# Performance work log

Hardware: AMD Instinct MI355X
Metric: run time of the kernel (lower is better)

Reference implementation:

```python
import jax, jax.numpy as jnp
import numpy as np

B, IN_UNITS, IN_CHANNELS, NUM_UNITS, UNIT_SIZE = 128, 32, 4096, 10, 16
NUM_ITER = 3


def setup_inputs() -> dict:
    key = jax.random.key(0)
    k1, k2 = jax.random.split(key)
    # x: primary-capsule output [B, in_units, in_channels]
    x = jax.random.normal(k1, (B, IN_UNITS, IN_CHANNELS), dtype=jnp.float32)
    # W: routing weights, torch param shape [1, C, J, D, K] with batch dim dropped
    W = jax.random.normal(k2, (IN_CHANNELS, NUM_UNITS, UNIT_SIZE, IN_UNITS), dtype=jnp.float32)
    return {"x": x, "W": W}


def reference(x, W):
    b_sz = x.shape[0]
    C, J = W.shape[0], W.shape[1]
    # torch: x.transpose(1,2) -> [B,C,K]; u_hat = W @ x -> [B,C,J,D,1]
    # u_hat[b,i,j,d] = sum_k W[i,j,d,k] * x[b,k,i]
    u_hat = jnp.einsum('ijdk,bki->bijd', W, x)  # [B, C, J, D]
    b_ij = jnp.zeros((C, J), dtype=x.dtype)
    v = None
    for _ in range(NUM_ITER):
        # faithful: softmax over dim=1 (in_channels axis), not over classes
        c_ij = jax.nn.softmax(b_ij, axis=0)               # [C, J]
        s = jnp.einsum('ij,bijd->bjd', c_ij, u_hat)        # [B, J, D]
        # faithful squash: original sums over dim=2 of [B,1,J,D,1] == class axis J
        mag_sq = jnp.sum(s * s, axis=1, keepdims=True)     # [B, 1, D]
        v = (mag_sq / (1.0 + mag_sq)) * (s / jnp.sqrt(mag_sq))
        # agreement: <u_hat, v> averaged over batch
        agree = jnp.einsum('bijd,bjd->ij', u_hat, v) / b_sz
        b_ij = b_ij + agree
    # torch returns v_j.squeeze(1): [B, J, D, 1]
    return v[:, :, :, None]
```

## Files before the change

### kernel.cpp

```cpp
#include <hip/hip_runtime.h>


typedef __attribute__((ext_vector_type(8))) __bf16 bf16x8;
typedef __attribute__((ext_vector_type(4))) float  f32x4;
typedef __attribute__((ext_vector_type(8))) unsigned short u16x8;
typedef __attribute__((ext_vector_type(4))) unsigned int  u32x4;

#define DI __device__ __forceinline__

DI float bf2f(unsigned short u){ unsigned int x = ((unsigned int)u) << 16; return __builtin_bit_cast(float, x); }
DI unsigned short f2bf(float f){
  unsigned int u = __builtin_bit_cast(unsigned int, f);
  u += 0x7fffu + ((u >> 16) & 1u);
  return (unsigned short)(u >> 16);
}
DI unsigned int cvtpk(float lo, float hi){
  unsigned int r;
  asm("v_cvt_pk_bf16_f32 %0, %1, %2" : "=v"(r) : "v"(lo), "v"(hi));
  return r;
}

constexpr int Ci = 4096, Kk = 32, Jj = 10, Dd = 16, Bb = 128;
constexpr int KI = Ci * Kk;
constexpr int JDt = Jj * Dd;
constexpr int NCH = 256, CK = 512;

constexpr size_t OFF_W2 = 0;
constexpr size_t SZ_W2  = (size_t)JDt * KI * 2;
constexpr size_t OFF_XT = OFF_W2 + SZ_W2;
constexpr size_t SZ_XT  = (size_t)KI * Bb * 2;
constexpr size_t OFF_BT = OFF_XT + SZ_XT;
constexpr size_t SZ_BT  = (size_t)Jj * Ci * 4;
constexpr size_t OFF_CT = OFF_BT + SZ_BT;
constexpr size_t OFF_VBT = OFF_CT + SZ_BT;
constexpr size_t SZ_VBT = (size_t)JDt * Bb * 2;
constexpr size_t OFF_SP = OFF_VBT + SZ_VBT;
constexpr size_t SZ_SP  = (size_t)NCH * Bb * JDt * 4;

__global__ __launch_bounds__(256) void pack_w(const float* __restrict__ W, unsigned short* __restrict__ w2){
  __shared__ float tile[128][65];
  const int mt = blockIdx.x % 80, it = blockIdx.x / 80;
  const int m0 = mt * 64, i0 = it * 128;
  #pragma unroll
  for(int u=0; u<8; u++){
    int e = threadIdx.x + 256*u;
    int il = e >> 4, q = e & 15;
    float4 v = *(const float4*)(W + (size_t)(i0+il)*5120 + m0 + q*4);
    tile[il][q*4+0]=v.x; tile[il][q*4+1]=v.y; tile[il][q*4+2]=v.z; tile[il][q*4+3]=v.w;
  }
  __syncthreads();
  #pragma unroll
  for(int u=0; u<4; u++){
    int e = threadIdx.x + 256*u;
    int ml = e >> 4, q = e & 15;
    u32x4 o;
    o[0]=cvtpk(tile[q*8+0][ml], tile[q*8+1][ml]);
    o[1]=cvtpk(tile[q*8+2][ml], tile[q*8+3][ml]);
    o[2]=cvtpk(tile[q*8+4][ml], tile[q*8+5][ml]);
    o[3]=cvtpk(tile[q*8+6][ml], tile[q*8+7][ml]);
    *(u32x4*)(w2 + (size_t)(m0+ml)*Ci + i0 + q*8) = o;
  }
}

__global__ __launch_bounds__(256) void pack_xt(const float* __restrict__ x, unsigned short* __restrict__ xT,
                                               float* __restrict__ bT){
  __shared__ float tile[128][65];
  const int bid = blockIdx.x;
  if(bid >= 2048){
    ((f32x4*)bT)[(bid-2048)*256 + threadIdx.x] = f32x4{0.f,0.f,0.f,0.f};
    return;
  }
  const int ki0 = bid * 64;
  #pragma unroll
  for(int u=0; u<8; u++){
    int e = threadIdx.x + 256*u;
    int bl = e >> 4, q = e & 15;
    float4 v = *(const float4*)(x + (size_t)bl*KI + ki0 + q*4);
    tile[bl][q*4+0]=v.x; tile[bl][q*4+1]=v.y; tile[bl][q*4+2]=v.z; tile[bl][q*4+3]=v.w;
  }
  __syncthreads();
  #pragma unroll
  for(int u=0; u<4; u++){
    int e = threadIdx.x + 256*u;
    int kil = e >> 4, g = e & 15;
    u32x4 o;
    o[0]=cvtpk(tile[g*8+0][kil], tile[g*8+1][kil]);
    o[1]=cvtpk(tile[g*8+2][kil], tile[g*8+3][kil]);
    o[2]=cvtpk(tile[g*8+4][kil], tile[g*8+5][kil]);
    o[3]=cvtpk(tile[g*8+6][kil], tile[g*8+7][kil]);
    *(u32x4*)(xT + (size_t)(ki0+kil)*Bb + g*8) = o;
  }
}

__global__ __launch_bounds__(256) void softmax_k(const float* __restrict__ bT, float* __restrict__ cT){
  const int j = blockIdx.x, tid = threadIdx.x, lane = tid & 63, wid = tid >> 6;
  __shared__ float red[4];
  float vals[16];
  float mx = -3.4e38f;
  #pragma unroll
  for(int u=0; u<16; u++){ vals[u] = bT[j*Ci + tid + 256*u]; mx = fmaxf(mx, vals[u]); }
  #pragma unroll
  for(int o=32; o>0; o>>=1) mx = fmaxf(mx, __shfl_xor(mx, o));
  if(lane == 0) red[wid] = mx;
  __syncthreads();
  mx = fmaxf(fmaxf(red[0],red[1]), fmaxf(red[2],red[3]));
  float sm = 0.f;
  #pragma unroll
  for(int u=0; u<16; u++){ vals[u] = expf(vals[u]-mx); sm += vals[u]; }
  #pragma unroll
  for(int o=32; o>0; o>>=1) sm += __shfl_xor(sm, o);
  __syncthreads();
  if(lane == 0) red[wid] = sm;
  __syncthreads();
  sm = red[0]+red[1]+red[2]+red[3];
  float inv = 1.0f / sm;
  #pragma unroll
  for(int u=0; u<16; u++) cT[j*Ci + tid + 256*u] = vals[u]*inv;
}

__global__ __launch_bounds__(512) void s_pass(const float* __restrict__ x,
                                              const unsigned short* __restrict__ w2,
                                              const float* __restrict__ cT,
                                              float* __restrict__ spart){
  __shared__ unsigned short xs[2][128*64];
  __shared__ unsigned short wsm[2][160*64];
  const int tid = threadIdx.x, lane = tid & 63, wid = tid >> 6;
  const int wb = wid & 3, wj = wid >> 2;
  const int ki0 = blockIdx.x * CK;
  const float cu = 1.0f/4096.0f;

  const int xb_ = tid >> 3, xsg = tid & 7;
  f32x4 acc[2][5];
  #pragma unroll
  for(int m=0;m<2;m++)
    #pragma unroll
    for(int n=0;n<5;n++) acc[m][n] = f32x4{0.f,0.f,0.f,0.f};

  float4 xv[4]; u16x8 wv[3]; float4 cv[3][2];

  #define S_LOAD(STEP) { \
    const int kb = ki0 + (STEP)*64; \
    const float* xr = x + (size_t)xb_*KI + kb + xsg*8; \
    xv[0]=*(const float4*)xr; xv[1]=*(const float4*)(xr+4); \
    const float* xr2 = xr + (size_t)64*KI; \
    xv[2]=*(const float4*)xr2; xv[3]=*(const float4*)(xr2+4); \
    const int ib = kb & (Ci-1); \
    _Pragma("unroll") \
    for(int u=0; u<3; u++){ int e = tid + 512*u; if(e < 1280){ \
      int jd = e>>3, sg = e&7; \
      wv[u] = *(const u16x8*)(w2 + (size_t)jd*KI + kb + sg*8); \
      if(cT){ const float* cp = cT + (jd>>4)*Ci + ib + sg*8; \
        cv[u][0] = *(const float4*)cp; cv[u][1] = *(const float4*)(cp+4); } \
    }} }

  #define S_WRITE(BUF) { \
    u32x4 xo; \
    xo[0]=cvtpk(xv[0].x,xv[0].y); xo[1]=cvtpk(xv[0].z,xv[0].w); \
    xo[2]=cvtpk(xv[1].x,xv[1].y); xo[3]=cvtpk(xv[1].z,xv[1].w); \
    *(u32x4*)((char*)xs[BUF] + xb_*128 + ((xsg*16) ^ ((xb_&7)<<4))) = xo; \
    xo[0]=cvtpk(xv[2].x,xv[2].y); xo[1]=cvtpk(xv[2].z,xv[2].w); \
    xo[2]=cvtpk(xv[3].x,xv[3].y); xo[3]=cvtpk(xv[3].z,xv[3].w); \
    *(u32x4*)((char*)xs[BUF] + (xb_+64)*128 + ((xsg*16) ^ ((xb_&7)<<4))) = xo; \
    _Pragma("unroll") \
    for(int u=0; u<3; u++){ int e = tid + 512*u; if(e < 1280){ \
      int jd = e>>3, sg = e&7; \
      float f[8]; \
      _Pragma("unroll") \
      for(int q=0;q<8;q++) f[q] = bf2f(wv[u][q]); \
      if(cT){ \
        f[0]*=cv[u][0].x; f[1]*=cv[u][0].y; f[2]*=cv[u][0].z; f[3]*=cv[u][0].w; \
        f[4]*=cv[u][1].x; f[5]*=cv[u][1].y; f[6]*=cv[u][1].z; f[7]*=cv[u][1].w; \
      } else { \
        _Pragma("unroll") \
        for(int q=0;q<8;q++) f[q] *= cu; \
      } \
      u32x4 wo; \
      wo[0]=cvtpk(f[0],f[1]); wo[1]=cvtpk(f[2],f[3]); \
      wo[2]=cvtpk(f[4],f[5]); wo[3]=cvtpk(f[6],f[7]); \
      *(u32x4*)((char*)wsm[BUF] + jd*128 + ((sg*16) ^ ((jd&7)<<4))) = wo; \
    }} }

  S_LOAD(0); S_WRITE(0);
  __syncthreads();
  int cur = 0;
  for(int step=0; step<8; ++step){
    if(step < 7) S_LOAD(step+1);
    #pragma unroll
    for(int ks=0; ks<2; ks++){
      const int kk2 = (ks*32 + ((lane>>4)<<3)) * 2;
      bf16x8 a[2];
      #pragma unroll
      for(int m=0;m<2;m++){
        int row = wb*32 + m*16 + (lane&15);
        a[m] = *(const bf16x8*)((const char*)xs[cur] + row*128 + (kk2 ^ ((row&7)<<4)));
      }
      #pragma unroll
      for(int n=0;n<5;n++){
        int row = wj*80 + n*16 + (lane&15);
        bf16x8 bb = *(const bf16x8*)((const char*)wsm[cur] + row*128 + (kk2 ^ ((row&7)<<4)));
        acc[0][n] = __builtin_amdgcn_mfma_f32_16x16x32_bf16(a[0], bb, acc[0][n], 0,0,0);
        acc[1][n] = __builtin_amdgcn_mfma_f32_16x16x32_bf16(a[1], bb, acc[1][n], 0,0,0);
      }
    }
    if(step < 7) S_WRITE(cur^1);
    __syncthreads();
    cur ^= 1;
  }
  float* sp = spart + (size_t)blockIdx.x * (Bb*JDt);
  #pragma unroll
  for(int m=0;m<2;m++)
    #pragma unroll
    for(int n=0;n<5;n++)
      #pragma unroll
      for(int r=0;r<4;r++){
        int b  = wb*32 + m*16 + ((lane>>4)<<2) + r;
        int jd = wj*80 + n*16 + (lane&15);
        sp[b*JDt + jd] = acc[m][n][r];
      }
}

__global__ __launch_bounds__(256) void redsq(const float* __restrict__ spart,
                                             float* __restrict__ vout,
                                             unsigned short* __restrict__ vbT){
  const int b = blockIdx.x, tid = threadIdx.x;
  __shared__ float sred[6][JDt];
  __shared__ float sq[JDt];
  __shared__ float scale[Dd];
  if(tid < 240){
    const int g = tid % 40, cg = tid / 40;
    f32x4 a = {0.f,0.f,0.f,0.f};
    for(int ch=cg; ch<NCH; ch+=6)
      a += *(const f32x4*)(spart + (size_t)ch*(Bb*JDt) + b*JDt + g*4);
    *(f32x4*)&sred[cg][g*4] = a;
  }
  __syncthreads();
  float s = 0.f;
  if(tid < JDt){
    #pragma unroll
    for(int c=0;c<6;c++) s += sred[c][tid];
    sq[tid] = s*s;
  }
  __syncthreads();
  if(tid < Dd){
    float m = 0.f;
    #pragma unroll
    for(int j=0;j<Jj;j++) m += sq[j*Dd + tid];
    scale[tid] = sqrtf(m) / (1.0f + m);
  }
  __syncthreads();
  if(tid < JDt){
    float v = s * scale[tid & (Dd-1)];
    vout[b*JDt + tid] = v;
    vbT[tid*Bb + b] = f2bf(v);
  }
}

__global__ __launch_bounds__(256) void agree_pass(const unsigned short* __restrict__ xT,
                                                  const unsigned short* __restrict__ vbT,
                                                  const unsigned short* __restrict__ w2,
                                                  float* __restrict__ bT){
  const int tid = threadIdx.x, lane = tid & 63, wid = tid >> 6;
  const int wj = wid & 1, wk = wid >> 1;
  const int ki0 = blockIdx.x * 64;
  const int bsl = (lane>>4)<<3;
  f32x4 acc[5][2];
  #pragma unroll
  for(int m=0;m<5;m++){ acc[m][0]=f32x4{0,0,0,0}; acc[m][1]=f32x4{0,0,0,0}; }
  #pragma unroll
  for(int ks=0; ks<4; ks++){
    bf16x8 af[5];
    #pragma unroll
    for(int m=0;m<5;m++){
      int jd = wj*80 + m*16 + (lane&15);
      af[m] = *(const bf16x8*)(vbT + jd*Bb + ks*32 + bsl);
    }
    #pragma unroll
    for(int n=0;n<2;n++){
      int kir = ki0 + wk*32 + n*16 + (lane&15);
      bf16x8 bf_ = *(const bf16x8*)(xT + (size_t)kir*Bb + ks*32 + bsl);
      #pragma unroll
      for(int m=0;m<5;m++)
        acc[m][n] = __builtin_amdgcn_mfma_f32_16x16x32_bf16(af[m], bf_, acc[m][n], 0,0,0);
    }
  }
  const int ibase = ki0 & (Ci-1);
  #pragma unroll
  for(int m=0;m<5;m++){
    int j = wj*5 + m;
    #pragma unroll
    for(int n=0;n<2;n++){
      int colg = ki0 + wk*32 + n*16 + (lane&15);
      float s = 0.f;
      #pragma unroll
      for(int r=0;r<4;r++){
        int jdrow = wj*80 + m*16 + ((lane>>4)<<2) + r;
        s += acc[m][n][r] * bf2f(w2[(size_t)jdrow*KI + colg]);
      }
      s += __shfl_xor(s, 16);
      s += __shfl_xor(s, 32);
      if(lane < 16){
        int ig = ibase + wk*32 + n*16 + lane;
        atomicAdd(bT + j*Ci + ig, s * (1.0f/128.0f));
      }
    }
  }
}

extern "C" void kernel_launch(void* const* d_in, const int* in_sizes, int n_in,
                              void* d_out, int out_size, void* d_ws, size_t ws_size,
                              hipStream_t stream) {
  const float* x = (const float*)d_in[0];
  const float* W = (const float*)d_in[1];
  float* out = (float*)d_out;
  char* ws = (char*)d_ws;
  unsigned short* w2  = (unsigned short*)(ws + OFF_W2);
  unsigned short* xT  = (unsigned short*)(ws + OFF_XT);
  float* bT           = (float*)(ws + OFF_BT);
  float* cT           = (float*)(ws + OFF_CT);
  unsigned short* vbT = (unsigned short*)(ws + OFF_VBT);
  float* spart        = (float*)(ws + OFF_SP);

  pack_w<<<2560, 256, 0, stream>>>(W, w2);
  pack_xt<<<2088, 256, 0, stream>>>(x, xT, bT);
  for(int t=0; t<3; t++){
    if(t > 0) softmax_k<<<Jj, 256, 0, stream>>>(bT, cT);
    s_pass<<<NCH, 512, 0, stream>>>(x, w2, (t==0)? nullptr : cT, spart);
    redsq<<<Bb, 256, 0, stream>>>(spart, out, vbT);
    if(t < 2) agree_pass<<<KI/64, 256, 0, stream>>>(xT, vbT, w2, bT);
  }
}
```

Before: 234.3 us.

## Pre-pack x to bf16, double s_pass grid, replace atomics with partial-sum reduce+softmax

pack_xt now also writes a row-major bf16 copy of x, so s_pass loads half the bytes and skips per-step conversion. s_pass runs twice as many blocks over shorter K chunks with occupancy hints, and its partials are stored batch-major. The cT loads move from the prefetch stage into the write stage to cut live registers. agree_pass writes per-slab partials instead of atomicAdd, and a new redsoft kernel fuses the slab reduction with the softmax. The cost is extra workspace, an extra bf16 x write, and a serial 32-slab reduction inside only 10 blocks.

```diff
diff --git a/kernel.cpp b/kernel.cpp
--- a/kernel.cpp
+++ b/kernel.cpp
@@ -23,19 +23,23 @@
 constexpr int Ci = 4096, Kk = 32, Jj = 10, Dd = 16, Bb = 128;
 constexpr int KI = Ci * Kk;
 constexpr int JDt = Jj * Dd;
-constexpr int NCH = 256, CK = 512;
+constexpr int NCH = 512, CK = 256;
 
 constexpr size_t OFF_W2 = 0;
 constexpr size_t SZ_W2  = (size_t)JDt * KI * 2;
 constexpr size_t OFF_XT = OFF_W2 + SZ_W2;
 constexpr size_t SZ_XT  = (size_t)KI * Bb * 2;
-constexpr size_t OFF_BT = OFF_XT + SZ_XT;
+constexpr size_t OFF_XB = OFF_XT + SZ_XT;
+constexpr size_t SZ_XB  = (size_t)Bb * KI * 2;
+constexpr size_t OFF_BT = OFF_XB + SZ_XB;
 constexpr size_t SZ_BT  = (size_t)Jj * Ci * 4;
 constexpr size_t OFF_CT = OFF_BT + SZ_BT;
 constexpr size_t OFF_VBT = OFF_CT + SZ_BT;
 constexpr size_t SZ_VBT = (size_t)JDt * Bb * 2;
-constexpr size_t OFF_SP = OFF_VBT + SZ_VBT;
-constexpr size_t SZ_SP  = (size_t)NCH * Bb * JDt * 4;
+constexpr size_t OFF_BP = OFF_VBT + SZ_VBT;
+constexpr size_t SZ_BP  = (size_t)Jj * Kk * Ci * 4;
+constexpr size_t OFF_SP = OFF_BP + SZ_BP;
+constexpr size_t SZ_SP  = (size_t)Bb * NCH * JDt * 4;
 
 __global__ __launch_bounds__(256) void pack_w(const float* __restrict__ W, unsigned short* __restrict__ w2){
   __shared__ float tile[128][65];
@@ -63,7 +67,7 @@
 }
 
 __global__ __launch_bounds__(256) void pack_xt(const float* __restrict__ x, unsigned short* __restrict__ xT,
-                                               float* __restrict__ bT){
+                                               unsigned short* __restrict__ xbf, float* __restrict__ bT){
   __shared__ float tile[128][65];
   const int bid = blockIdx.x;
   if(bid >= 2048){
@@ -90,38 +94,23 @@
     o[3]=cvtpk(tile[g*8+6][kil], tile[g*8+7][kil]);
     *(u32x4*)(xT + (size_t)(ki0+kil)*Bb + g*8) = o;
   }
-}
-
-__global__ __launch_bounds__(256) void softmax_k(const float* __restrict__ bT, float* __restrict__ cT){
-  const int j = blockIdx.x, tid = threadIdx.x, lane = tid & 63, wid = tid >> 6;
-  __shared__ float red[4];
-  float vals[16];
-  float mx = -3.4e38f;
-  #pragma unroll
-  for(int u=0; u<16; u++){ vals[u] = bT[j*Ci + tid + 256*u]; mx = fmaxf(mx, vals[u]); }
-  #pragma unroll
-  for(int o=32; o>0; o>>=1) mx = fmaxf(mx, __shfl_xor(mx, o));
-  if(lane == 0) red[wid] = mx;
-  __syncthreads();
-  mx = fmaxf(fmaxf(red[0],red[1]), fmaxf(red[2],red[3]));
-  float sm = 0.f;
-  #pragma unroll
-  for(int u=0; u<16; u++){ vals[u] = expf(vals[u]-mx); sm += vals[u]; }
-  #pragma unroll
-  for(int o=32; o>0; o>>=1) sm += __shfl_xor(sm, o);
-  __syncthreads();
-  if(lane == 0) red[wid] = sm;
-  __syncthreads();
-  sm = red[0]+red[1]+red[2]+red[3];
-  float inv = 1.0f / sm;
-  #pragma unroll
-  for(int u=0; u<16; u++) cT[j*Ci + tid + 256*u] = vals[u]*inv;
-}
-
-__global__ __launch_bounds__(512) void s_pass(const float* __restrict__ x,
-                                              const unsigned short* __restrict__ w2,
-                                              const float* __restrict__ cT,
-                                              float* __restrict__ spart){
+  #pragma unroll
+  for(int u=0; u<4; u++){
+    int e = threadIdx.x + 256*u;
+    int row = e >> 3, sg = e & 7;
+    u32x4 o;
+    o[0]=cvtpk(tile[row][sg*8+0], tile[row][sg*8+1]);
+    o[1]=cvtpk(tile[row][sg*8+2], tile[row][sg*8+3]);
+    o[2]=cvtpk(tile[row][sg*8+4], tile[row][sg*8+5]);
+    o[3]=cvtpk(tile[row][sg*8+6], tile[row][sg*8+7]);
+    *(u32x4*)(xbf + (size_t)row*KI + ki0 + sg*8) = o;
+  }
+}
+
+__global__ __launch_bounds__(512, 4) void s_pass(const unsigned short* __restrict__ xbf,
+                                                 const unsigned short* __restrict__ w2,
+                                                 const float* __restrict__ cT,
+                                                 float* __restrict__ spart){
   __shared__ unsigned short xs[2][128*64];
   __shared__ unsigned short wsm[2][160*64];
   const int tid = threadIdx.x, lane = tid & 63, wid = tid >> 6;
@@ -136,31 +125,22 @@
     #pragma unroll
     for(int n=0;n<5;n++) acc[m][n] = f32x4{0.f,0.f,0.f,0.f};
 
-  float4 xv[4]; u16x8 wv[3]; float4 cv[3][2];
+  u16x8 xv0, xv1; u16x8 wv[3]; int ibn;
 
   #define S_LOAD(STEP) { \
     const int kb = ki0 + (STEP)*64; \
-    const float* xr = x + (size_t)xb_*KI + kb + xsg*8; \
-    xv[0]=*(const float4*)xr; xv[1]=*(const float4*)(xr+4); \
-    const float* xr2 = xr + (size_t)64*KI; \
-    xv[2]=*(const float4*)xr2; xv[3]=*(const float4*)(xr2+4); \
-    const int ib = kb & (Ci-1); \
+    xv0 = *(const u16x8*)(xbf + (size_t)xb_*KI + kb + xsg*8); \
+    xv1 = *(const u16x8*)(xbf + (size_t)(xb_+64)*KI + kb + xsg*8); \
+    ibn = kb & (Ci-1); \
     _Pragma("unroll") \
     for(int u=0; u<3; u++){ int e = tid + 512*u; if(e < 1280){ \
       int jd = e>>3, sg = e&7; \
       wv[u] = *(const u16x8*)(w2 + (size_t)jd*KI + kb + sg*8); \
-      if(cT){ const float* cp = cT + (jd>>4)*Ci + ib + sg*8; \
-        cv[u][0] = *(const float4*)cp; cv[u][1] = *(const float4*)(cp+4); } \
     }} }
 
   #define S_WRITE(BUF) { \
-    u32x4 xo; \
-    xo[0]=cvtpk(xv[0].x,xv[0].y); xo[1]=cvtpk(xv[0].z,xv[0].w); \
-    xo[2]=cvtpk(xv[1].x,xv[1].y); xo[3]=cvtpk(xv[1].z,xv[1].w); \
-    *(u32x4*)((char*)xs[BUF] + xb_*128 + ((xsg*16) ^ ((xb_&7)<<4))) = xo; \
-    xo[0]=cvtpk(xv[2].x,xv[2].y); xo[1]=cvtpk(xv[2].z,xv[2].w); \
-    xo[2]=cvtpk(xv[3].x,xv[3].y); xo[3]=cvtpk(xv[3].z,xv[3].w); \
-    *(u32x4*)((char*)xs[BUF] + (xb_+64)*128 + ((xsg*16) ^ ((xb_&7)<<4))) = xo; \
+    *(u16x8*)((char*)xs[BUF] + xb_*128 + ((xsg*16) ^ ((xb_&7)<<4))) = xv0; \
+    *(u16x8*)((char*)xs[BUF] + (xb_+64)*128 + ((xsg*16) ^ ((xb_&7)<<4))) = xv1; \
     _Pragma("unroll") \
     for(int u=0; u<3; u++){ int e = tid + 512*u; if(e < 1280){ \
       int jd = e>>3, sg = e&7; \
@@ -168,8 +148,10 @@
       _Pragma("unroll") \
       for(int q=0;q<8;q++) f[q] = bf2f(wv[u][q]); \
       if(cT){ \
-        f[0]*=cv[u][0].x; f[1]*=cv[u][0].y; f[2]*=cv[u][0].z; f[3]*=cv[u][0].w; \
-        f[4]*=cv[u][1].x; f[5]*=cv[u][1].y; f[6]*=cv[u][1].z; f[7]*=cv[u][1].w; \
+        const float* cp = cT + (jd>>4)*Ci + ibn + sg*8; \
+        float4 c0 = *(const float4*)cp; float4 c1 = *(const float4*)(cp+4); \
+        f[0]*=c0.x; f[1]*=c0.y; f[2]*=c0.z; f[3]*=c0.w; \
+        f[4]*=c1.x; f[5]*=c1.y; f[6]*=c1.z; f[7]*=c1.w; \
       } else { \
         _Pragma("unroll") \
         for(int q=0;q<8;q++) f[q] *= cu; \
@@ -183,8 +165,8 @@
   S_LOAD(0); S_WRITE(0);
   __syncthreads();
   int cur = 0;
-  for(int step=0; step<8; ++step){
-    if(step < 7) S_LOAD(step+1);
+  for(int step=0; step<4; ++step){
+    if(step < 3) S_LOAD(step+1);
     #pragma unroll
     for(int ks=0; ks<2; ks++){
       const int kk2 = (ks*32 + ((lane>>4)<<3)) * 2;
@@ -202,11 +184,10 @@
         acc[1][n] = __builtin_amdgcn_mfma_f32_16x16x32_bf16(a[1], bb, acc[1][n], 0,0,0);
       }
     }
-    if(step < 7) S_WRITE(cur^1);
+    if(step < 3) S_WRITE(cur^1);
     __syncthreads();
     cur ^= 1;
   }
-  float* sp = spart + (size_t)blockIdx.x * (Bb*JDt);
   #pragma unroll
   for(int m=0;m<2;m++)
     #pragma unroll
@@ -215,7 +196,7 @@
       for(int r=0;r<4;r++){
         int b  = wb*32 + m*16 + ((lane>>4)<<2) + r;
         int jd = wj*80 + n*16 + (lane&15);
-        sp[b*JDt + jd] = acc[m][n][r];
+        spart[(size_t)b*(NCH*JDt) + blockIdx.x*JDt + jd] = acc[m][n][r];
       }
 }
 
@@ -226,15 +207,16 @@
   __shared__ float sred[6][JDt];
   __shared__ float sq[JDt];
   __shared__ float scale[Dd];
+  float s = 0.f;
   if(tid < 240){
     const int g = tid % 40, cg = tid / 40;
+    const float* p = spart + (size_t)b*(NCH*JDt);
     f32x4 a = {0.f,0.f,0.f,0.f};
     for(int ch=cg; ch<NCH; ch+=6)
-      a += *(const f32x4*)(spart + (size_t)ch*(Bb*JDt) + b*JDt + g*4);
+      a += *(const f32x4*)(p + ch*JDt + g*4);
     *(f32x4*)&sred[cg][g*4] = a;
   }
   __syncthreads();
-  float s = 0.f;
   if(tid < JDt){
     #pragma unroll
     for(int c=0;c<6;c++) s += sred[c][tid];
@@ -258,7 +240,7 @@
 __global__ __launch_bounds__(256) void agree_pass(const unsigned short* __restrict__ xT,
                                                   const unsigned short* __restrict__ vbT,
                                                   const unsigned short* __restrict__ w2,
-                                                  float* __restrict__ bT){
+                                                  float* __restrict__ bTp){
   const int tid = threadIdx.x, lane = tid & 63, wid = tid >> 6;
   const int wj = wid & 1, wk = wid >> 1;
   const int ki0 = blockIdx.x * 64;
@@ -284,6 +266,7 @@
     }
   }
   const int ibase = ki0 & (Ci-1);
+  const int kslab = ki0 >> 12;
   #pragma unroll
   for(int m=0;m<5;m++){
     int j = wj*5 + m;
@@ -300,9 +283,51 @@
       s += __shfl_xor(s, 32);
       if(lane < 16){
         int ig = ibase + wk*32 + n*16 + lane;
-        atomicAdd(bT + j*Ci + ig, s * (1.0f/128.0f));
-      }
-    }
+        bTp[(size_t)j*(Kk*Ci) + kslab*Ci + ig] = s * (1.0f/128.0f);
+      }
+    }
+  }
+}
+
+__global__ __launch_bounds__(256) void redsoft(const float* __restrict__ bTp,
+                                               float* __restrict__ bT, float* __restrict__ cT){
+  const int j = blockIdx.x, tid = threadIdx.x, lane = tid & 63, wid = tid >> 6;
+  __shared__ float red[4];
+  f32x4 a[4];
+  #pragma unroll
+  for(int g=0; g<4; g++) a[g] = *(const f32x4*)(bT + j*Ci + tid*16 + g*4);
+  for(int k=0; k<Kk; k++){
+    const float* p = bTp + (size_t)j*(Kk*Ci) + k*Ci + tid*16;
+    #pragma unroll
+    for(int g=0; g<4; g++) a[g] += *(const f32x4*)(p + g*4);
+  }
+  float mx = -3.4e38f;
+  #pragma unroll
+  for(int g=0; g<4; g++)
+    #pragma unroll
+    for(int c=0; c<4; c++) mx = fmaxf(mx, a[g][c]);
+  #pragma unroll
+  for(int o=32; o>0; o>>=1) mx = fmaxf(mx, __shfl_xor(mx, o));
+  if(lane == 0) red[wid] = mx;
+  __syncthreads();
+  mx = fmaxf(fmaxf(red[0],red[1]), fmaxf(red[2],red[3]));
+  float e[16]; float sm = 0.f;
+  #pragma unroll
+  for(int g=0; g<4; g++)
+    #pragma unroll
+    for(int c=0; c<4; c++){ e[g*4+c] = expf(a[g][c]-mx); sm += e[g*4+c]; }
+  #pragma unroll
+  for(int o=32; o>0; o>>=1) sm += __shfl_xor(sm, o);
+  __syncthreads();
+  if(lane == 0) red[wid] = sm;
+  __syncthreads();
+  sm = red[0]+red[1]+red[2]+red[3];
+  float inv = 1.0f / sm;
+  #pragma unroll
+  for(int g=0; g<4; g++){
+    *(f32x4*)(bT + j*Ci + tid*16 + g*4) = a[g];
+    f32x4 o; o[0]=e[g*4]*inv; o[1]=e[g*4+1]*inv; o[2]=e[g*4+2]*inv; o[3]=e[g*4+3]*inv;
+    *(f32x4*)(cT + j*Ci + tid*16 + g*4) = o;
   }
 }
 
@@ -315,17 +340,21 @@
   char* ws = (char*)d_ws;
   unsigned short* w2  = (unsigned short*)(ws + OFF_W2);
   unsigned short* xT  = (unsigned short*)(ws + OFF_XT);
+  unsigned short* xbf = (unsigned short*)(ws + OFF_XB);
   float* bT           = (float*)(ws + OFF_BT);
   float* cT           = (float*)(ws + OFF_CT);
   unsigned short* vbT = (unsigned short*)(ws + OFF_VBT);
+  float* bTp          = (float*)(ws + OFF_BP);
   float* spart        = (float*)(ws + OFF_SP);
 
   pack_w<<<2560, 256, 0, stream>>>(W, w2);
-  pack_xt<<<2088, 256, 0, stream>>>(x, xT, bT);
+  pack_xt<<<2088, 256, 0, stream>>>(x, xT, xbf, bT);
   for(int t=0; t<3; t++){
-    if(t > 0) softmax_k<<<Jj, 256, 0, stream>>>(bT, cT);
-    s_pass<<<NCH, 512, 0, stream>>>(x, w2, (t==0)? nullptr : cT, spart);
+    s_pass<<<NCH, 512, 0, stream>>>(xbf, w2, (t==0)? nullptr : cT, spart);
     redsq<<<Bb, 256, 0, stream>>>(spart, out, vbT);
-    if(t < 2) agree_pass<<<KI/64, 256, 0, stream>>>(xT, vbT, w2, bT);
-  }
-}
+    if(t < 2){
+      agree_pass<<<KI/64, 256, 0, stream>>>(xT, vbT, w2, bTp);
+      redsoft<<<Jj, 256, 0, stream>>>(bTp, bT, cT);
+    }
+  }
+}
```

Result: slower. 277.4 us (+18.4%).

## Pre-pack x to bf16 once and reshape pack kernels for wider tiles

Applied to the files above, without the earlier changes.

pack_xt now also writes a row-major bf16 copy of x, which s_pass reads in each of its three passes instead of loading fp32 x and converting it. pack_w is retiled to 512-thread blocks that convert to bf16 before the shared-memory transpose, which halves the LDS footprint per element. s_pass also defers the cT loads from the prefetch stage to the write stage to reduce register pressure. The cost is an extra bf16 buffer in the workspace and an extra write pass over x, and the cT loads are no longer hidden behind the MFMA loop.

```diff
diff --git a/kernel.cpp b/kernel.cpp
--- a/kernel.cpp
+++ b/kernel.cpp
@@ -29,7 +29,9 @@
 constexpr size_t SZ_W2  = (size_t)JDt * KI * 2;
 constexpr size_t OFF_XT = OFF_W2 + SZ_W2;
 constexpr size_t SZ_XT  = (size_t)KI * Bb * 2;
-constexpr size_t OFF_BT = OFF_XT + SZ_XT;
+constexpr size_t OFF_XB = OFF_XT + SZ_XT;
+constexpr size_t SZ_XB  = (size_t)Bb * KI * 2;
+constexpr size_t OFF_BT = OFF_XB + SZ_XB;
 constexpr size_t SZ_BT  = (size_t)Jj * Ci * 4;
 constexpr size_t OFF_CT = OFF_BT + SZ_BT;
 constexpr size_t OFF_VBT = OFF_CT + SZ_BT;
@@ -37,58 +39,75 @@
 constexpr size_t OFF_SP = OFF_VBT + SZ_VBT;
 constexpr size_t SZ_SP  = (size_t)NCH * Bb * JDt * 4;
 
-__global__ __launch_bounds__(256) void pack_w(const float* __restrict__ W, unsigned short* __restrict__ w2){
-  __shared__ float tile[128][65];
-  const int mt = blockIdx.x % 80, it = blockIdx.x / 80;
-  const int m0 = mt * 64, i0 = it * 128;
+constexpr int WPAD = 522;
+__global__ __launch_bounds__(512) void pack_w(const float* __restrict__ W, unsigned short* __restrict__ w2){
+  __shared__ unsigned short t16[64 * WPAD];
+  const int mt = blockIdx.x % 10, it = blockIdx.x / 10;
+  const int m0 = mt * 512, i0 = it * 64;
+  #pragma unroll
+  for(int u=0; u<16; u++){
+    int e = threadIdx.x + 512*u;
+    int row = e >> 7, c4 = e & 127;
+    float4 v = *(const float4*)(W + (size_t)(i0+row)*5120 + m0 + c4*4);
+    unsigned int* p = (unsigned int*)(t16 + row*WPAD + c4*4);
+    p[0] = cvtpk(v.x, v.y);
+    p[1] = cvtpk(v.z, v.w);
+  }
+  __syncthreads();
   #pragma unroll
   for(int u=0; u<8; u++){
-    int e = threadIdx.x + 256*u;
-    int il = e >> 4, q = e & 15;
-    float4 v = *(const float4*)(W + (size_t)(i0+il)*5120 + m0 + q*4);
-    tile[il][q*4+0]=v.x; tile[il][q*4+1]=v.y; tile[il][q*4+2]=v.z; tile[il][q*4+3]=v.w;
-  }
-  __syncthreads();
-  #pragma unroll
-  for(int u=0; u<4; u++){
-    int e = threadIdx.x + 256*u;
-    int ml = e >> 4, q = e & 15;
+    int e = threadIdx.x + 512*u;
+    int mr = e >> 3, g = e & 7;
     u32x4 o;
-    o[0]=cvtpk(tile[q*8+0][ml], tile[q*8+1][ml]);
-    o[1]=cvtpk(tile[q*8+2][ml], tile[q*8+3][ml]);
-    o[2]=cvtpk(tile[q*8+4][ml], tile[q*8+5][ml]);
-    o[3]=cvtpk(tile[q*8+6][ml], tile[q*8+7][ml]);
-    *(u32x4*)(w2 + (size_t)(m0+ml)*Ci + i0 + q*8) = o;
-  }
-}
-
+    #pragma unroll
+    for(int j=0; j<4; j++){
+      unsigned int lo = t16[(g*8 + 2*j    )*WPAD + mr];
+      unsigned int hi = t16[(g*8 + 2*j + 1)*WPAD + mr];
+      o[j] = lo | (hi << 16);
+    }
+    *(u32x4*)(w2 + (size_t)(m0+mr)*Ci + i0 + g*8) = o;
+  }
+}
+
+constexpr int XPAD = 134;
 __global__ __launch_bounds__(256) void pack_xt(const float* __restrict__ x, unsigned short* __restrict__ xT,
-                                               float* __restrict__ bT){
-  __shared__ float tile[128][65];
+                                               unsigned short* __restrict__ xbf, float* __restrict__ bT){
+  __shared__ float tile[64 * XPAD];
   const int bid = blockIdx.x;
   if(bid >= 2048){
     ((f32x4*)bT)[(bid-2048)*256 + threadIdx.x] = f32x4{0.f,0.f,0.f,0.f};
     return;
   }
-  const int ki0 = bid * 64;
+  const int ki0 = (bid >> 1) * 128, b0 = (bid & 1) * 64;
   #pragma unroll
   for(int u=0; u<8; u++){
     int e = threadIdx.x + 256*u;
-    int bl = e >> 4, q = e & 15;
-    float4 v = *(const float4*)(x + (size_t)bl*KI + ki0 + q*4);
-    tile[bl][q*4+0]=v.x; tile[bl][q*4+1]=v.y; tile[bl][q*4+2]=v.z; tile[bl][q*4+3]=v.w;
+    int row = e >> 5, q = e & 31;
+    float4 v = *(const float4*)(x + (size_t)(b0+row)*KI + ki0 + q*4);
+    float2* p = (float2*)(tile + row*XPAD + q*4);
+    p[0] = float2{v.x, v.y};
+    p[1] = float2{v.z, v.w};
   }
   __syncthreads();
   #pragma unroll
   for(int u=0; u<4; u++){
     int e = threadIdx.x + 256*u;
-    int kil = e >> 4, g = e & 15;
+    int kir = e >> 3, g = e & 7;
     u32x4 o;
-    o[0]=cvtpk(tile[g*8+0][kil], tile[g*8+1][kil]);
-    o[1]=cvtpk(tile[g*8+2][kil], tile[g*8+3][kil]);
-    o[2]=cvtpk(tile[g*8+4][kil], tile[g*8+5][kil]);
-    o[3]=cvtpk(tile[g*8+6][kil], tile[g*8+7][kil]);
-    *(u32x4*)(xT + (size_t)(ki0+kil)*Bb + g*8) = o;
+    #pragma unroll
+    for(int j=0; j<4; j++)
+      o[j] = cvtpk(tile[(g*8 + 2*j)*XPAD + kir], tile[(g*8 + 2*j + 1)*XPAD + kir]);
+    *(u32x4*)(xT + (size_t)(ki0+kir)*Bb + b0 + g*8) = o;
+  }
+  #pragma unroll
+  for(int u=0; u<4; u++){
+    int e = threadIdx.x + 256*u;
+    int row = e >> 4, sg = e & 15;
+    u32x4 o;
+    #pragma unroll
+    for(int j=0; j<4; j++)
+      o[j] = cvtpk(tile[row*XPAD + sg*8 + 2*j], tile[row*XPAD + sg*8 + 2*j + 1]);
+    *(u32x4*)(xbf + (size_t)(b0+row)*KI + ki0 + sg*8) = o;
   }
 }
 
@@ -118,7 +137,7 @@
   for(int u=0; u<16; u++) cT[j*Ci + tid + 256*u] = vals[u]*inv;
 }
 
-__global__ __launch_bounds__(512) void s_pass(const float* __restrict__ x,
+__global__ __launch_bounds__(512) void s_pass(const unsigned short* __restrict__ xbf,
                                               const unsigned short* __restrict__ w2,
                                               const float* __restrict__ cT,
                                               float* __restrict__ spart){
@@ -136,31 +155,22 @@
     #pragma unroll
     for(int n=0;n<5;n++) acc[m][n] = f32x4{0.f,0.f,0.f,0.f};
 
-  float4 xv[4]; u16x8 wv[3]; float4 cv[3][2];
+  u16x8 xv0, xv1; u16x8 wv[3]; int ibn;
 
   #define S_LOAD(STEP) { \
     const int kb = ki0 + (STEP)*64; \
-    const float* xr = x + (size_t)xb_*KI + kb + xsg*8; \
-    xv[0]=*(const float4*)xr; xv[1]=*(const float4*)(xr+4); \
-    const float* xr2 = xr + (size_t)64*KI; \
-    xv[2]=*(const float4*)xr2; xv[3]=*(const float4*)(xr2+4); \
-    const int ib = kb & (Ci-1); \
+    xv0 = *(const u16x8*)(xbf + (size_t)xb_*KI + kb + xsg*8); \
+    xv1 = *(const u16x8*)(xbf + (size_t)(xb_+64)*KI + kb + xsg*8); \
+    ibn = kb & (Ci-1); \
     _Pragma("unroll") \
     for(int u=0; u<3; u++){ int e = tid + 512*u; if(e < 1280){ \
       int jd = e>>3, sg = e&7; \
       wv[u] = *(const u16x8*)(w2 + (size_t)jd*KI + kb + sg*8); \
-      if(cT){ const float* cp = cT + (jd>>4)*Ci + ib + sg*8; \
-        cv[u][0] = *(const float4*)cp; cv[u][1] = *(const float4*)(cp+4); } \
     }} }
 
   #define S_WRITE(BUF) { \
-    u32x4 xo; \
-    xo[0]=cvtpk(xv[0].x,xv[0].y); xo[1]=cvtpk(xv[0].z,xv[0].w); \
-    xo[2]=cvtpk(xv[1].x,xv[1].y); xo[3]=cvtpk(xv[1].z,xv[1].w); \
-    *(u32x4*)((char*)xs[BUF] + xb_*128 + ((xsg*16) ^ ((xb_&7)<<4))) = xo; \
-    xo[0]=cvtpk(xv[2].x,xv[2].y); xo[1]=cvtpk(xv[2].z,xv[2].w); \
-    xo[2]=cvtpk(xv[3].x,xv[3].y); xo[3]=cvtpk(xv[3].z,xv[3].w); \
-    *(u32x4*)((char*)xs[BUF] + (xb_+64)*128 + ((xsg*16) ^ ((xb_&7)<<4))) = xo; \
+    *(u16x8*)((char*)xs[BUF] + xb_*128 + ((xsg*16) ^ ((xb_&7)<<4))) = xv0; \
+    *(u16x8*)((char*)xs[BUF] + (xb_+64)*128 + ((xsg*16) ^ ((xb_&7)<<4))) = xv1; \
     _Pragma("unroll") \
     for(int u=0; u<3; u++){ int e = tid + 512*u; if(e < 1280){ \
       int jd = e>>3, sg = e&7; \
@@ -168,8 +178,10 @@
       _Pragma("unroll") \
       for(int q=0;q<8;q++) f[q] = bf2f(wv[u][q]); \
       if(cT){ \
-        f[0]*=cv[u][0].x; f[1]*=cv[u][0].y; f[2]*=cv[u][0].z; f[3]*=cv[u][0].w; \
-        f[4]*=cv[u][1].x; f[5]*=cv[u][1].y; f[6]*=cv[u][1].z; f[7]*=cv[u][1].w; \
+        const float* cp = cT + (jd>>4)*Ci + ibn + sg*8; \
+        float4 c0 = *(const float4*)cp; float4 c1 = *(const float4*)(cp+4); \
+        f[0]*=c0.x; f[1]*=c0.y; f[2]*=c0.z; f[3]*=c0.w; \
+        f[4]*=c1.x; f[5]*=c1.y; f[6]*=c1.z; f[7]*=c1.w; \
       } else { \
         _Pragma("unroll") \
         for(int q=0;q<8;q++) f[q] *= cu; \
@@ -226,6 +238,7 @@
   __shared__ float sred[6][JDt];
   __shared__ float sq[JDt];
   __shared__ float scale[Dd];
+  float s = 0.f;
   if(tid < 240){
     const int g = tid % 40, cg = tid / 40;
     f32x4 a = {0.f,0.f,0.f,0.f};
@@ -234,7 +247,6 @@
     *(f32x4*)&sred[cg][g*4] = a;
   }
   __syncthreads();
-  float s = 0.f;
   if(tid < JDt){
     #pragma unroll
     for(int c=0;c<6;c++) s += sred[c][tid];
@@ -315,16 +327,17 @@
   char* ws = (char*)d_ws;
   unsigned short* w2  = (unsigned short*)(ws + OFF_W2);
   unsigned short* xT  = (unsigned short*)(ws + OFF_XT);
+  unsigned short* xbf = (unsigned short*)(ws + OFF_XB);
   float* bT           = (float*)(ws + OFF_BT);
   float* cT           = (float*)(ws + OFF_CT);
   unsigned short* vbT = (unsigned short*)(ws + OFF_VBT);
   float* spart        = (float*)(ws + OFF_SP);
 
-  pack_w<<<2560, 256, 0, stream>>>(W, w2);
-  pack_xt<<<2088, 256, 0, stream>>>(x, xT, bT);
+  pack_w<<<640, 512, 0, stream>>>(W, w2);
+  pack_xt<<<2088, 256, 0, stream>>>(x, xT, xbf, bT);
   for(int t=0; t<3; t++){
     if(t > 0) softmax_k<<<Jj, 256, 0, stream>>>(bT, cT);
-    s_pass<<<NCH, 512, 0, stream>>>(x, w2, (t==0)? nullptr : cT, spart);
+    s_pass<<<NCH, 512, 0, stream>>>(xbf, w2, (t==0)? nullptr : cT, spart);
     redsq<<<Bb, 256, 0, stream>>>(spart, out, vbT);
     if(t < 2) agree_pass<<<KI/64, 256, 0, stream>>>(xT, vbT, w2, bT);
   }
```

Result: slower. 240.3 us (+2.6%).
